# Optimization experiments

Measured on AMD Instinct MI355X. Metric: run time of the kernel, lower is better.

The kernel has to match this reference:

```python
import jax, jax.numpy as jnp
import numpy as np

LEAKY_ALPHA = 0.2  # tf.nn.leaky_relu default

def setup_inputs() -> dict:
    key = jax.random.key(0)
    k1, k2, k3 = jax.random.split(key, 3)
    B, N, F, U = 4, 4096, 128, 64
    x = jax.random.normal(k1, (B, N, F), dtype=jnp.float32)
    W = jax.random.normal(k2, (F, U), dtype=jnp.float32) * (1.0 / np.sqrt(F))
    a = jax.random.normal(k3, (2 * U, 1), dtype=jnp.float32) * (1.0 / np.sqrt(2 * U))
    return {"x": x, "W": W, "a": a}

def reference(x, W, a):
    # h: (B, N, U)
    h = jnp.einsum('bnf,fu->bnu', x, W)
    U = h.shape[-1]
    a1 = a[:U, 0]   # attends to source node i
    a2 = a[U:, 0]   # attends to target node j
    # a^T [h_i || h_j] = a1^T h_i + a2^T h_j  (same math, no O(N^2*2U) concat)
    f1 = jnp.einsum('bnu,u->bn', h, a1)  # (B, N)
    f2 = jnp.einsum('bnu,u->bn', h, a2)  # (B, N)
    e = f1[:, :, None] + f2[:, None, :]  # (B, N, N)
    e = jnp.where(e >= 0, e, LEAKY_ALPHA * e)
    attn = jax.nn.softmax(e, axis=-1)    # softmax over j
    return jnp.einsum('bij,bju->biu', attn, h)
```

## Files before the change

### kernel.cpp

```cpp
#include <hip/hip_runtime.h>
#include <hip/hip_bf16.h>

#define NBATCH 4
#define NN 4096
#define NF 128
#define NU 64
#define CH 16
#define NCH (NN / CH)
#define LEAKY 0.2f

__global__ __launch_bounds__(256) void k1_h(
    const float* __restrict__ x, const float* __restrict__ W,
    const float* __restrict__ a,
    float* __restrict__ h, float* __restrict__ f1, float* __restrict__ f2) {
  __shared__ float xs[16][NF];
  int tid = threadIdx.x;
  int row0 = blockIdx.x * 16;
  const float4* xg = (const float4*)(x + (size_t)row0 * NF);
  float4* xs4 = (float4*)xs;
  for (int k = tid; k < 16 * NF / 4; k += 256) xs4[k] = xg[k];
  __syncthreads();
  int u = tid & 63;
  int wv = tid >> 6;
  float acc[4] = {0.f, 0.f, 0.f, 0.f};
#pragma unroll 4
  for (int f = 0; f < NF; f += 4) {
    float w0 = W[(f+0)*NU+u], w1 = W[(f+1)*NU+u],
          w2 = W[(f+2)*NU+u], w3 = W[(f+3)*NU+u];
#pragma unroll
    for (int r = 0; r < 4; ++r) {
      float4 xv = *(const float4*)&xs[wv*4+r][f];
      acc[r] += xv.x*w0 + xv.y*w1 + xv.z*w2 + xv.w*w3;
    }
  }
  float a1 = a[u], a2 = a[NU+u];
#pragma unroll
  for (int r = 0; r < 4; ++r) {
    int grow = row0 + wv*4 + r;
    h[(size_t)grow*NU+u] = acc[r];
    float p1 = acc[r]*a1, p2 = acc[r]*a2;
#pragma unroll
    for (int off = 32; off >= 1; off >>= 1) {
      p1 += __shfl_xor(p1, off, 64);
      p2 += __shfl_xor(p2, off, 64);
    }
    if (u == 0) { f1[grow] = p1; f2[grow] = p2; }
  }
}

__global__ __launch_bounds__(256) void k2a_count(
    const float* __restrict__ f2, unsigned short* __restrict__ pc) {
  __shared__ float fsk[256];
  int b = blockIdx.x >> 8;
  int jc = (blockIdx.x >> 4) & 15;
  int kc = blockIdx.x & 15;
  int tid = threadIdx.x;
  const float* f2b = f2 + b * NN;
  fsk[tid] = f2b[kc * 256 + tid];
  __syncthreads();
  int j = jc * 256 + tid;
  float my = f2b[j];
  int lim = j - kc * 256;
  int cnt = 0;
#pragma unroll 8
  for (int k = 0; k < 256; ++k) {
    float v = fsk[k];
    cnt += (v < my) || (v == my && k < lim);
  }
  pc[((size_t)(b * 16 + kc)) * NN + j] = (unsigned short)cnt;
}

__global__ __launch_bounds__(256) void k2b_scatter(
    const float* __restrict__ f2, const unsigned short* __restrict__ pc,
    float4* __restrict__ sdat, float* __restrict__ f2s) {
  int b = blockIdx.x >> 4;
  int jc = blockIdx.x & 15;
  int j = jc * 256 + threadIdx.x;
  float my = f2[b * NN + j];
  int rank = 0;
#pragma unroll
  for (int kc = 0; kc < 16; ++kc)
    rank += pc[((size_t)(b * 16 + kc)) * NN + j];
  int o = b * NN + rank;
  float4 v;
  v.x = my; v.y = expf(my); v.z = expf(LEAKY * my); v.w = __int_as_float(j);
  sdat[o] = v;
  f2s[o] = my;
}

__global__ __launch_bounds__(256) void k3_csum(
    const float* __restrict__ h, const float4* __restrict__ sdat,
    float* __restrict__ Pvhi, float* __restrict__ Pvlo,
    float* __restrict__ Pshi, float* __restrict__ Pslo) {
  int u = threadIdx.x & 63;
  int wv = threadIdx.x >> 6;
  int cg = blockIdx.x * 4 + wv;
  int b = cg >> 8;
  int c = cg & (NCH - 1);
  int k0 = b * NN + c * CH;
  const float* hb = h + (size_t)b * NN * NU;
  float ah = 0.f, al = 0.f, sh = 0.f, sl = 0.f;
#pragma unroll
  for (int k = 0; k < CH; ++k) {
    float4 e = sdat[k0 + k];
    int j = __float_as_int(e.w);
    float hv = hb[(size_t)j * NU + u];
    ah += e.y * hv; al += e.z * hv; sh += e.y; sl += e.z;
  }
  size_t o = (size_t)(b * (NCH + 1) + c) * NU + u;
  Pvhi[o] = ah; Pvlo[o] = al;
  if (u == 0) { Pshi[b * (NCH + 1) + c] = sh; Pslo[b * (NCH + 1) + c] = sl; }
}

__global__ __launch_bounds__(256) void k3b_scan(
    float* __restrict__ Pvhi, float* __restrict__ Pvlo,
    float* __restrict__ Pshi, float* __restrict__ Pslo) {
  int wid = blockIdx.x * 4 + (threadIdx.x >> 6);
  int l = threadIdx.x & 63;
  if (wid < 512) {
    int b = wid >> 7;
    int half = (wid >> 6) & 1;
    int u = wid & 63;
    float* T = half ? Pvlo : Pvhi;
    size_t i0 = (size_t)(b * (NCH + 1) + 4 * l) * NU + u;
    float v0 = T[i0], v1 = T[i0 + NU], v2 = T[i0 + 2*NU], v3 = T[i0 + 3*NU];
    float lsum = v0 + v1 + v2 + v3, s = lsum;
#pragma unroll
    for (int off = 1; off < 64; off <<= 1) {
      float t = __shfl_up(s, off, 64);
      if (l >= off) s += t;
    }
    float e = s - lsum;
    T[i0] = e;
    T[i0 + NU] = e + v0;
    T[i0 + 2*NU] = e + v0 + v1;
    T[i0 + 3*NU] = e + v0 + v1 + v2;
    if (l == 63) T[(size_t)(b * (NCH + 1) + NCH) * NU + u] = s;
  } else if (wid < 520) {
    int s2 = wid - 512;
    int b = s2 >> 1;
    float* T = (s2 & 1) ? Pslo : Pshi;
    int i0 = b * (NCH + 1) + 4 * l;
    float v0 = T[i0], v1 = T[i0 + 1], v2 = T[i0 + 2], v3 = T[i0 + 3];
    float lsum = v0 + v1 + v2 + v3, s = lsum;
#pragma unroll
    for (int off = 1; off < 64; off <<= 1) {
      float t = __shfl_up(s, off, 64);
      if (l >= off) s += t;
    }
    float e = s - lsum;
    T[i0] = e; T[i0 + 1] = e + v0; T[i0 + 2] = e + v0 + v1;
    T[i0 + 3] = e + v0 + v1 + v2;
    if (l == 63) T[b * (NCH + 1) + NCH] = s;
  }
}

__global__ __launch_bounds__(256) void k4_out(
    const float* __restrict__ f1, const float* __restrict__ f2s,
    const float* __restrict__ h, const float4* __restrict__ sdat,
    const float* __restrict__ Pvhi, const float* __restrict__ Pvlo,
    const float* __restrict__ Pshi, const float* __restrict__ Pslo,
    float* __restrict__ out) {
  int u = threadIdx.x & 63;
  int wv = threadIdx.x >> 6;
  int row = blockIdx.x * 4 + wv;
  int b = row >> 12;
  const float* fs = f2s + b * NN;
  float fv = f1[row];
  float theta = -fv;
  float q1 = fs[u * 64 + 63];
  int n1 = __popcll(__ballot(q1 < theta));
  int t;
  if (n1 == 64) {
    t = NN;
  } else {
    float q2 = fs[n1 * 64 + u];
    t = n1 * 64 + __popcll(__ballot(q2 < theta));
  }
  int c = t >> 4; if (c > NCH - 1) c = NCH - 1;
  int k0 = b * NN + c * CH;
  const float* hb = h + (size_t)b * NN * NU;
  float ch = 0.f, cl = 0.f, csh = 0.f, csl = 0.f;
#pragma unroll
  for (int k = 0; k < CH; ++k) {
    int kg = c * CH + k;
    float4 e = sdat[k0 + k];
    int j = __float_as_int(e.w);
    float hv = hb[(size_t)j * NU + u];
    bool hi = (kg >= t);
    float wH = hi ? e.y : 0.f;
    float wL = hi ? 0.f : e.z;
    ch += wH * hv; cl += wL * hv; csh += wH; csl += wL;
  }
  size_t base = (size_t)b * (NCH + 1);
  size_t oc0 = (base + c) * NU + u;
  size_t oc1 = (base + c + 1) * NU + u;
  size_t oT  = (base + NCH) * NU + u;
  float Ahi = (Pvhi[oT] - Pvhi[oc1]) + ch;
  float Alo = Pvlo[oc0] + cl;
  float Shi = (Pshi[base + NCH] - Pshi[base + c + 1]) + csh;
  float Slo = Pslo[base + c] + csl;
  float e1 = expf(fv), e1l = expf(LEAKY * fv);
  float den = e1 * Shi + e1l * Slo;
  out[(size_t)row * NU + u] = (e1 * Ahi + e1l * Alo) / den;
}

extern "C" void kernel_launch(void* const* d_in, const int* in_sizes, int n_in,
                              void* d_out, int out_size, void* d_ws, size_t ws_size,
                              hipStream_t stream) {
  const float* x = (const float*)d_in[0];
  const float* W = (const float*)d_in[1];
  const float* a = (const float*)d_in[2];
  float* out = (float*)d_out;
  float* ws = (float*)d_ws;

  size_t o = 0;
  float* h    = ws + o; o += (size_t)NBATCH * NN * NU;
  float* f1   = ws + o; o += (size_t)NBATCH * NN;
  float* f2   = ws + o; o += (size_t)NBATCH * NN;
  float* f2s  = ws + o; o += (size_t)NBATCH * NN;
  float4* sdat = (float4*)(ws + o); o += (size_t)NBATCH * NN * 4;
  float* Pvhi = ws + o; o += (size_t)NBATCH * (NCH + 1) * NU;
  float* Pvlo = ws + o; o += (size_t)NBATCH * (NCH + 1) * NU;
  float* Pshi = ws + o; o += (size_t)NBATCH * (NCH + 1);
  float* Pslo = ws + o; o += (size_t)NBATCH * (NCH + 1);
  unsigned short* pc = (unsigned short*)(ws + o); o += (size_t)NBATCH * 16 * NN / 2;

  k1_h<<<(NBATCH * NN) / 16, 256, 0, stream>>>(x, W, a, h, f1, f2);
  k2a_count<<<NBATCH * 256, 256, 0, stream>>>(f2, pc);
  k2b_scatter<<<NBATCH * 16, 256, 0, stream>>>(f2, pc, sdat, f2s);
  k3_csum<<<(NBATCH * NCH) / 4, 256, 0, stream>>>(h, sdat, Pvhi, Pvlo, Pshi, Pslo);
  k3b_scan<<<130, 256, 0, stream>>>(Pvhi, Pvlo, Pshi, Pslo);
  k4_out<<<(NBATCH * NN) / 4, 256, 0, stream>>>(f1, f2s, h, sdat,
      Pvhi, Pvlo, Pshi, Pslo, out);
}
```

Before: 108.2 us.

## Fuse rank counting and scatter into one kernel with in-block count reduction

Merges the two-pass rank sort (partial counts written to global, then summed and scattered) into a single kernel. Each block handles 64 keys, with four waves each counting against a quarter of every 1024-element shared tile, then reducing the counts in shared memory before scattering. This drops one launch and the global partial-count buffer, and reads the comparison values as float4. In exchange there are only 256 blocks, each looping over all 4096 keys, so parallelism per block is lower and only one wave does the final scatter.

```diff
diff --git a/kernel.cpp b/kernel.cpp
--- a/kernel.cpp
+++ b/kernel.cpp
@@ -48,44 +48,48 @@
   }
 }
 
-__global__ __launch_bounds__(256) void k2a_count(
-    const float* __restrict__ f2, unsigned short* __restrict__ pc) {
-  __shared__ float fsk[256];
-  int b = blockIdx.x >> 8;
-  int jc = (blockIdx.x >> 4) & 15;
-  int kc = blockIdx.x & 15;
+__global__ __launch_bounds__(256) void k2_ranksc(
+    const float* __restrict__ f2, float4* __restrict__ sdat,
+    float* __restrict__ f2s) {
+  __shared__ float fsk[1024];
+  __shared__ unsigned short cnts[4][64];
+  int b = blockIdx.x >> 6;
+  int jc = blockIdx.x & 63;
   int tid = threadIdx.x;
+  int lane = tid & 63;
+  int wv = tid >> 6;
   const float* f2b = f2 + b * NN;
-  fsk[tid] = f2b[kc * 256 + tid];
+  int j = jc * 64 + lane;
+  float my = f2b[j];
+  int cnt = 0;
+  for (int kc = 0; kc < 4; ++kc) {
+    __syncthreads();
+    for (int k = tid; k < 1024; k += 256) fsk[k] = f2b[kc * 1024 + k];
+    __syncthreads();
+    int k0g = kc * 1024 + wv * 256;
+    const float* base = &fsk[wv * 256];
+#pragma unroll 8
+    for (int k = 0; k < 256; k += 4) {
+      float4 v = *(const float4*)&base[k];
+      int kg = k0g + k;
+      cnt += (v.x < my) || (v.x == my && kg + 0 < j);
+      cnt += (v.y < my) || (v.y == my && kg + 1 < j);
+      cnt += (v.z < my) || (v.z == my && kg + 2 < j);
+      cnt += (v.w < my) || (v.w == my && kg + 3 < j);
+    }
+  }
+  cnts[wv][lane] = (unsigned short)cnt;
   __syncthreads();
-  int j = jc * 256 + tid;
-  float my = f2b[j];
-  int lim = j - kc * 256;
-  int cnt = 0;
-#pragma unroll 8
-  for (int k = 0; k < 256; ++k) {
-    float v = fsk[k];
-    cnt += (v < my) || (v == my && k < lim);
-  }
-  pc[((size_t)(b * 16 + kc)) * NN + j] = (unsigned short)cnt;
-}
-
-__global__ __launch_bounds__(256) void k2b_scatter(
-    const float* __restrict__ f2, const unsigned short* __restrict__ pc,
-    float4* __restrict__ sdat, float* __restrict__ f2s) {
-  int b = blockIdx.x >> 4;
-  int jc = blockIdx.x & 15;
-  int j = jc * 256 + threadIdx.x;
-  float my = f2[b * NN + j];
-  int rank = 0;
-#pragma unroll
-  for (int kc = 0; kc < 16; ++kc)
-    rank += pc[((size_t)(b * 16 + kc)) * NN + j];
-  int o = b * NN + rank;
-  float4 v;
-  v.x = my; v.y = expf(my); v.z = expf(LEAKY * my); v.w = __int_as_float(j);
-  sdat[o] = v;
-  f2s[o] = my;
+  if (tid < 64) {
+    int rank = cnts[0][tid] + cnts[1][tid] + cnts[2][tid] + cnts[3][tid];
+    int jj = jc * 64 + tid;
+    float v = f2b[jj];
+    int o = b * NN + rank;
+    float4 e;
+    e.x = v; e.y = expf(v); e.z = expf(LEAKY * v); e.w = __int_as_float(jj);
+    sdat[o] = e;
+    f2s[o] = v;
+  }
 }
 
 __global__ __launch_bounds__(256) void k3_csum(
@@ -224,11 +228,9 @@
   float* Pvlo = ws + o; o += (size_t)NBATCH * (NCH + 1) * NU;
   float* Pshi = ws + o; o += (size_t)NBATCH * (NCH + 1);
   float* Pslo = ws + o; o += (size_t)NBATCH * (NCH + 1);
-  unsigned short* pc = (unsigned short*)(ws + o); o += (size_t)NBATCH * 16 * NN / 2;
 
   k1_h<<<(NBATCH * NN) / 16, 256, 0, stream>>>(x, W, a, h, f1, f2);
-  k2a_count<<<NBATCH * 256, 256, 0, stream>>>(f2, pc);
-  k2b_scatter<<<NBATCH * 16, 256, 0, stream>>>(f2, pc, sdat, f2s);
+  k2_ranksc<<<NBATCH * 64, 256, 0, stream>>>(f2, sdat, f2s);
   k3_csum<<<(NBATCH * NCH) / 4, 256, 0, stream>>>(h, sdat, Pvhi, Pvlo, Pshi, Pslo);
   k3b_scan<<<130, 256, 0, stream>>>(Pvhi, Pvlo, Pshi, Pslo);
   k4_out<<<(NBATCH * NN) / 4, 256, 0, stream>>>(f1, f2s, h, sdat,
```

Result: slower. 123.9 us (+14.5%).
